# Kernel optimization log

Measured on AMD Instinct MI355X. Metric: run time of the kernel, lower is better.

Reference implementation:

```python
import jax, jax.numpy as jnp
import numpy as np

D_MODEL = 1024
N_HEADS = 16
HEAD_DIM = D_MODEL // N_HEADS
FFN_DIM = 4096
T = 2048
LN_EPS = 1e-5


def layer_norm(x, g, b):
    mu = jnp.mean(x, axis=-1, keepdims=True)
    var = jnp.mean(jnp.square(x - mu), axis=-1, keepdims=True)
    return (x - mu) * jax.lax.rsqrt(var + LN_EPS) * g + b


def setup_inputs() -> dict:
    key = jax.random.key(0)
    ks = jax.random.split(key, 12)
    s = 0.02
    x = jax.random.normal(ks[0], (1, T, D_MODEL), dtype=jnp.float32)
    # causal mask: True means masked (strict upper triangle)
    causal_mask = jnp.triu(jnp.ones((T, T), dtype=bool), k=1)
    # ALiBi bias: -slope * distance, per head
    slopes = 2.0 ** (-8.0 * (jnp.arange(1, N_HEADS + 1, dtype=jnp.float32) / N_HEADS))
    pos = jnp.arange(T, dtype=jnp.float32)
    dist = pos[None, :] - pos[:, None]  # (T, T)
    alibi_bias = slopes[:, None, None] * jnp.minimum(dist, 0.0)[None]  # (H, T, T)
    inp = {
        "x": x,
        "causal_mask": causal_mask,
        "alibi_bias": alibi_bias.astype(jnp.float32),
        "wq": jax.random.normal(ks[1], (D_MODEL, D_MODEL), jnp.float32) * s,
        "bq": jnp.zeros((D_MODEL,), jnp.float32),
        "wk": jax.random.normal(ks[2], (D_MODEL, D_MODEL), jnp.float32) * s,
        "bk": jnp.zeros((D_MODEL,), jnp.float32),
        "wv": jax.random.normal(ks[3], (D_MODEL, D_MODEL), jnp.float32) * s,
        "bv": jnp.zeros((D_MODEL,), jnp.float32),
        "wo": jax.random.normal(ks[4], (D_MODEL, D_MODEL), jnp.float32) * s,
        "bo": jnp.zeros((D_MODEL,), jnp.float32),
        "w1": jax.random.normal(ks[5], (D_MODEL, FFN_DIM), jnp.float32) * s,
        "b1": jnp.zeros((FFN_DIM,), jnp.float32),
        "w2": jax.random.normal(ks[6], (FFN_DIM, D_MODEL), jnp.float32) * s,
        "b2": jnp.zeros((D_MODEL,), jnp.float32),
        "g1": jnp.ones((D_MODEL,), jnp.float32),
        "be1": jnp.zeros((D_MODEL,), jnp.float32),
        "g2": jnp.ones((D_MODEL,), jnp.float32),
        "be2": jnp.zeros((D_MODEL,), jnp.float32),
    }
    return inp


def reference(x, causal_mask, alibi_bias, wq, bq, wk, bk, wv, bv, wo, bo,
              w1, b1, w2, b2, g1, be1, g2, be2):
    B, Tt, D = x.shape
    H, hd = N_HEADS, HEAD_DIM
    x_norm = layer_norm(x, g1, be1)
    # projections -> (B, H, T, hd)
    def split_heads(y):
        return y.reshape(B, Tt, H, hd).transpose(0, 2, 1, 3)
    Q = split_heads(x_norm @ wq + bq)
    K = split_heads(x_norm @ wk + bk)
    V = split_heads(x_norm @ wv + bv)
    scale = jnp.sqrt(jnp.float32(hd))
    scores = jnp.einsum('bhqd,bhkd->bhqk', Q, K) / scale
    scores = scores + alibi_bias[None]
    scores = jnp.where(causal_mask[None, None], -jnp.inf, scores)
    attn = jax.nn.softmax(scores, axis=-1)
    attn_out = jnp.einsum('bhqk,bhkd->bhqd', attn, V)
    attn_out = attn_out.transpose(0, 2, 1, 3).reshape(B, Tt, D)
    attn_out = attn_out @ wo + bo
    x = x + attn_out
    x_norm = layer_norm(x, g2, be2)
    h = jax.nn.gelu(x_norm @ w1 + b1, approximate=False)
    ffn_out = h @ w2 + b2
    return x + ffn_out
```

## Files before the change

kernel.cpp:

```cpp
#include <hip/hip_runtime.h>
#include <hip/hip_bf16.h>
#include <math.h>

#define T_SEQ 2048
#define D_MODEL 1024
#define N_HEADS 16
#define HEAD_DIM 64
#define FFN_DIM 4096

typedef _Float16 halfx8 __attribute__((ext_vector_type(8)));
typedef _Float16 halfx4 __attribute__((ext_vector_type(4)));
typedef float floatx4 __attribute__((ext_vector_type(4)));

__device__ __forceinline__ void async_ld16(const _Float16* g, _Float16* l) {
  __builtin_amdgcn_global_load_lds(
      (const __attribute__((address_space(1))) unsigned int*)g,
      (__attribute__((address_space(3))) unsigned int*)l, 16, 0, 0);
}

template <int N> __device__ __forceinline__ void wait_barrier();
template <> __device__ __forceinline__ void wait_barrier<0>() {
  asm volatile("s_waitcnt vmcnt(0)\n\ts_barrier" ::: "memory");
}
template <> __device__ __forceinline__ void wait_barrier<2>() {
  asm volatile("s_waitcnt vmcnt(2)\n\ts_barrier" ::: "memory");
}
template <> __device__ __forceinline__ void wait_barrier<3>() {
  asm volatile("s_waitcnt vmcnt(3)\n\ts_barrier" ::: "memory");
}
template <> __device__ __forceinline__ void wait_barrier<4>() {
  asm volatile("s_waitcnt vmcnt(4)\n\ts_barrier" ::: "memory");
}

#define DPP_STEP(v, CTRL, OP)                                                 \
  {                                                                           \
    float _t = __int_as_float(__builtin_amdgcn_update_dpp(                    \
        0, __float_as_int(v), CTRL, 0xF, 0xF, true));                         \
    (v) = OP((v), _t);                                                        \
  }
#define OP_MAXF(a, b) fmaxf((a), (b))
#define OP_ADDF(a, b) ((a) + (b))

__global__ __launch_bounds__(256) void prep_ln_kernel(
    const float* __restrict__ wq, const float* __restrict__ wk,
    const float* __restrict__ wv, const float* __restrict__ wo,
    const float* __restrict__ w1, const float* __restrict__ w2,
    const float* __restrict__ bq, const float* __restrict__ bk,
    const float* __restrict__ bv, _Float16* __restrict__ Wqkvt,
    _Float16* __restrict__ Wot, _Float16* __restrict__ W1t,
    _Float16* __restrict__ W2t, float* __restrict__ bqkv,
    const float* __restrict__ x, const float* __restrict__ g1,
    const float* __restrict__ be1, _Float16* __restrict__ xnh) {
  int bId = blockIdx.x;
  int tid = threadIdx.x;
  if (bId >= 12300) {
    int row = bId - 12300;
    const float* xr = x + (size_t)row * D_MODEL;
    _Float16* yr = xnh + (size_t)row * D_MODEL;
    int lid = tid & 63, wid = tid >> 6;
    __shared__ float red[8];
    float4 v = *(const float4*)&xr[tid * 4];
    float sum = v.x + v.y + v.z + v.w;
    for (int o = 32; o > 0; o >>= 1) sum += __shfl_down(sum, o, 64);
    if (lid == 0) red[wid] = sum;
    __syncthreads();
    if (tid == 0) { float t = 0; for (int i = 0; i < 4; i++) t += red[i]; red[0] = t; }
    __syncthreads();
    float mu = red[0] * (1.0f / D_MODEL);
    __syncthreads();
    float dx = v.x - mu, dy = v.y - mu, dz = v.z - mu, dw = v.w - mu;
    float vs = dx * dx + dy * dy + dz * dz + dw * dw;
    for (int o = 32; o > 0; o >>= 1) vs += __shfl_down(vs, o, 64);
    if (lid == 0) red[wid] = vs;
    __syncthreads();
    if (tid == 0) { float t = 0; for (int i = 0; i < 4; i++) t += red[i]; red[0] = t; }
    __syncthreads();
    float rstd = rsqrtf(red[0] * (1.0f / D_MODEL) + 1e-5f);
    float4 gv = *(const float4*)&g1[tid * 4];
    float4 bv4 = *(const float4*)&be1[tid * 4];
    halfx4 o;
    o[0] = (_Float16)(dx * rstd * gv.x + bv4.x);
    o[1] = (_Float16)(dy * rstd * gv.y + bv4.y);
    o[2] = (_Float16)(dz * rstd * gv.z + bv4.z);
    o[3] = (_Float16)(dw * rstd * gv.w + bv4.w);
    *(halfx4*)&yr[tid * 4] = o;
    return;
  }
  if (bId >= 12288) {
    int i = (bId - 12288) * 256 + tid;
    if (i < 1024) bqkv[i] = bq[i];
    else if (i < 2048) bqkv[i] = bk[i - 1024];
    else bqkv[i] = bv[i - 2048];
    return;
  }
  const float* in; _Float16* outp; int K, N, t;
  if (bId < 1024)      { in = wq; outp = Wqkvt;                 K = 1024; N = 1024; t = bId; }
  else if (bId < 2048) { in = wk; outp = Wqkvt + 1024 * 1024;   K = 1024; N = 1024; t = bId - 1024; }
  else if (bId < 3072) { in = wv; outp = Wqkvt + 2 * 1024 * 1024; K = 1024; N = 1024; t = bId - 2048; }
  else if (bId < 4096) { in = wo; outp = Wot;                   K = 1024; N = 1024; t = bId - 3072; }
  else if (bId < 8192) { in = w1; outp = W1t;                   K = 1024; N = 4096; t = bId - 4096; }
  else                 { in = w2; outp = W2t;                   K = 4096; N = 1024; t = bId - 8192; }
  int ntn = N / 32;
  int tk = (t / ntn) * 32, tn = (t % ntn) * 32;

  __shared__ float tile[32][33];
  int r = tid >> 3, c = (tid & 7) * 4;
  float4 v = *(const float4*)&in[(size_t)(tk + r) * N + tn + c];
  tile[r][c] = v.x; tile[r][c + 1] = v.y; tile[r][c + 2] = v.z; tile[r][c + 3] = v.w;
  __syncthreads();
  halfx4 o;
  o[0] = (_Float16)tile[c][r];
  o[1] = (_Float16)tile[c + 1][r];
  o[2] = (_Float16)tile[c + 2][r];
  o[3] = (_Float16)tile[c + 3][r];
  *(halfx4*)&outp[(size_t)(tn + r) * K + tk + c] = o;
}

__global__ __launch_bounds__(256) void ln_h_kernel(
    const float* __restrict__ x, const float* __restrict__ g,
    const float* __restrict__ b, _Float16* __restrict__ y) {
  int row = blockIdx.x;
  const float* xr = x + (size_t)row * D_MODEL;
  _Float16* yr = y + (size_t)row * D_MODEL;
  int tid = threadIdx.x;
  int lid = tid & 63, wid = tid >> 6;
  __shared__ float red[8];

  float4 v = *(const float4*)&xr[tid * 4];
  float sum = v.x + v.y + v.z + v.w;
  for (int o = 32; o > 0; o >>= 1) sum += __shfl_down(sum, o, 64);
  if (lid == 0) red[wid] = sum;
  __syncthreads();
  if (tid == 0) { float t = 0; for (int i = 0; i < 4; i++) t += red[i]; red[0] = t; }
  __syncthreads();
  float mu = red[0] * (1.0f / D_MODEL);
  __syncthreads();

  float dx = v.x - mu, dy = v.y - mu, dz = v.z - mu, dw = v.w - mu;
  float vs = dx * dx + dy * dy + dz * dz + dw * dw;
  for (int o = 32; o > 0; o >>= 1) vs += __shfl_down(vs, o, 64);
  if (lid == 0) red[wid] = vs;
  __syncthreads();
  if (tid == 0) { float t = 0; for (int i = 0; i < 4; i++) t += red[i]; red[0] = t; }
  __syncthreads();
  float rstd = rsqrtf(red[0] * (1.0f / D_MODEL) + 1e-5f);

  float4 gv = *(const float4*)&g[tid * 4];
  float4 bv = *(const float4*)&b[tid * 4];
  halfx4 o;
  o[0] = (_Float16)(dx * rstd * gv.x + bv.x);
  o[1] = (_Float16)(dy * rstd * gv.y + bv.y);
  o[2] = (_Float16)(dz * rstd * gv.z + bv.z);
  o[3] = (_Float16)(dw * rstd * gv.w + bv.w);
  *(halfx4*)&yr[tid * 4] = o;
}

template <int MODE, int BM, int BN>
__global__ __launch_bounds__(256) void hgemm_kernel(
    const _Float16* __restrict__ A, const _Float16* __restrict__ Bt,
    const float* __restrict__ bias, const float* __restrict__ res,
    float* __restrict__ Cf, _Float16* __restrict__ Ch,
    _Float16* __restrict__ Vtg, int M, int N, int K) {
  constexpr int TM = BM / 32;
  constexpr int TN = BN / 32;
  constexpr int AR = BM / 64;
  constexpr int BR = BN / 64;
  constexpr int L = AR + BR;
  __shared__ _Float16 As[3][BM][32];
  __shared__ _Float16 Bs[3][BN][32];
  const int tid = threadIdx.x;
  const int w = tid >> 6, lane = tid & 63;
  const int l16 = lane & 15, quad = lane >> 4;
  const int m0 = blockIdx.y * BM, n0 = blockIdx.x * BN;
  const int wm = (w >> 1) * (BM / 2), wn = (w & 1) * (BN / 2);

  floatx4 acc[TM][TN];
#pragma unroll
  for (int i = 0; i < TM; i++)
#pragma unroll
    for (int j = 0; j < TN; j++) acc[i][j] = (floatx4){0.f, 0.f, 0.f, 0.f};

  const int srow = w * 16 + (lane >> 2);
  const int gg = (lane & 3) ^ ((srow >> 1) & 3);
  const _Float16* Agp = A + (size_t)(m0 + srow) * K + gg * 8;
  const _Float16* Bgp = Bt + (size_t)(n0 + srow) * K + gg * 8;

  const int colA = (quad ^ ((l16 >> 1) & 3)) * 8;

  const int NIT = K / 32;
#define HG_ISSUE(buf, k0)                                                     \
  {                                                                           \
    _Pragma("unroll") for (int i = 0; i < AR; i++)                            \
        async_ld16(Agp + (k0) + (size_t)i * 64 * K, &As[buf][i * 64 + w * 16][0]); \
    _Pragma("unroll") for (int i = 0; i < BR; i++)                            \
        async_ld16(Bgp + (k0) + (size_t)i * 64 * K, &Bs[buf][i * 64 + w * 16][0]); \
  }
  HG_ISSUE(0, 0)
  HG_ISSUE(1, 32)

  for (int it = 0; it < NIT; it++) {
    const int buf = it % 3;
    if (it + 1 < NIT) wait_barrier<L>();
    else wait_barrier<0>();
    if (it + 2 < NIT) HG_ISSUE((it + 2) % 3, (it + 2) * 32)
    halfx8 af[TM], bf[TN];
#pragma unroll
    for (int mt = 0; mt < TM; mt++)
      af[mt] = *(const halfx8*)&As[buf][wm + mt * 16 + l16][colA];
#pragma unroll
    for (int nt = 0; nt < TN; nt++)
      bf[nt] = *(const halfx8*)&Bs[buf][wn + nt * 16 + l16][colA];
#pragma unroll
    for (int mt = 0; mt < TM; mt++)
#pragma unroll
      for (int nt = 0; nt < TN; nt++)
        acc[mt][nt] = __builtin_amdgcn_mfma_f32_16x16x32_f16(af[mt], bf[nt], acc[mt][nt], 0, 0, 0);
  }

#pragma unroll
  for (int mt = 0; mt < TM; mt++) {
    int row0 = m0 + wm + mt * 16 + quad * 4;
#pragma unroll
    for (int nt = 0; nt < TN; nt++) {
      int col = n0 + wn + nt * 16 + l16;
      float bv = bias[col];
      float vv[4];
#pragma unroll
      for (int r = 0; r < 4; r++) {
        float v = acc[mt][nt][r] + bv;
        if (MODE == 1) v = 0.5f * v * (1.0f + erff(v * 0.70710678118f));
        vv[r] = v;
      }
      if (MODE == 2) {
#pragma unroll
        for (int r = 0; r < 4; r++)
          Cf[(size_t)(row0 + r) * N + col] = vv[r] + res[(size_t)(row0 + r) * N + col];
      } else if (MODE == 3) {
        if (col < 2048) {
#pragma unroll
          for (int r = 0; r < 4; r++)
            Ch[(size_t)(row0 + r) * 2048 + col] = (_Float16)vv[r];
        } else {
          halfx4 pk;
#pragma unroll
          for (int r = 0; r < 4; r++) pk[r] = (_Float16)vv[r];
          *(halfx4*)&Vtg[(size_t)(col - 2048) * T_SEQ + row0] = pk;
        }
      } else {
#pragma unroll
        for (int r = 0; r < 4; r++)
          Ch[(size_t)(row0 + r) * N + col] = (_Float16)vv[r];
      }
    }
  }
}

#define LROW 72
__global__ __launch_bounds__(256) void flash_attn_kernel(
    const _Float16* __restrict__ QK, const _Float16* __restrict__ Vtg,
    _Float16* __restrict__ out) {
  __shared__ _Float16 Ks[2][64][64];
  __shared__ _Float16 Vt[2][64][64];
  __shared__ _Float16 Ps[4][16][LROW];

  const int h = blockIdx.y;
  const int qt = 31 - blockIdx.x;
  const int q0 = qt * 64;
  const int tid = threadIdx.x;
  const int w = tid >> 6;
  const int lane = tid & 63;
  const int l16 = lane & 15;
  const int quad = lane >> 4;

  const _Float16* Qg = QK + h * HEAD_DIM;
  const _Float16* Kg = QK + 1024 + h * HEAD_DIM;
  const _Float16* Vg = Vtg + (size_t)h * HEAD_DIM * T_SEQ;

  const _Float16* qp = Qg + (size_t)(q0 + w * 16 + l16) * 2048;
  halfx8 qa0 = *(const halfx8*)(qp + quad * 8);
  halfx8 qa1 = *(const halfx8*)(qp + 32 + quad * 8);

  const float scale2 = 0.18033688f;
  const float slope2 = exp2f(-0.5f * (float)(h + 1)) * 1.44269504f;
  const int row_base = q0 + w * 16 + quad * 4;

  const int sr = w * 8 + (lane >> 3);
  const int gg = (lane & 7) ^ ((lane >> 3) & 7);
  const _Float16* Kp = Kg + (size_t)sr * 2048 + gg * 8;
  const _Float16* Vp = Vg + (size_t)sr * 2048 + gg * 8;

  const int m7 = l16 & 7;
  const int cK0 = (quad ^ m7) * 8;
  const int cK1 = cK0 ^ 32;
  const int cV0 = (quad ^ m7) * 8;
  const int cV1 = ((quad + 4) ^ m7) * 8;

#define FA_ISSUE(buf, k0)                                                      \
  {                                                                            \
    async_ld16(Kp + (size_t)(k0) * 2048, &Ks[buf][w * 8][0]);                  \
    async_ld16(Kp + (size_t)((k0) + 32) * 2048, &Ks[buf][32 + w * 8][0]);      \
    async_ld16(Vp + (k0), &Vt[buf][w * 8][0]);                                 \
    async_ld16(Vp + (size_t)32 * 2048 + (k0), &Vt[buf][32 + w * 8][0]);        \
  }

  float m_i[4], l_i[4];
  floatx4 o_acc[4];
#pragma unroll
  for (int r = 0; r < 4; r++) { m_i[r] = -INFINITY; l_i[r] = 0.f; }
#pragma unroll
  for (int c = 0; c < 4; c++) o_acc[c] = (floatx4){0.f, 0.f, 0.f, 0.f};

  FA_ISSUE(0, 0)

  for (int t = 0; t <= qt; t++) {
    const int k0 = t * 64;
    const int buf = t & 1;
    wait_barrier<0>();
    if (t < qt) FA_ISSUE(buf ^ 1, k0 + 64)

    float sc[4][4];
#pragma unroll
    for (int sub = 0; sub < 4; sub++) {
      const _Float16* kr = &Ks[buf][sub * 16 + l16][0];
      halfx8 b0 = *(const halfx8*)(kr + cK0);
      halfx8 b1 = *(const halfx8*)(kr + cK1);
      floatx4 acc = (floatx4){0.f, 0.f, 0.f, 0.f};
      acc = __builtin_amdgcn_mfma_f32_16x16x32_f16(qa0, b0, acc, 0, 0, 0);
      acc = __builtin_amdgcn_mfma_f32_16x16x32_f16(qa1, b1, acc, 0, 0, 0);
#pragma unroll
      for (int r = 0; r < 4; r++) sc[sub][r] = acc[r];
    }

    const bool diag = (t == qt);
    float mx[4];
#pragma unroll
    for (int r = 0; r < 4; r++) {
      const int rg = row_base + r;
      float ab = slope2 * (float)(k0 + l16 - rg);
      mx[r] = m_i[r];
#pragma unroll
      for (int sub = 0; sub < 4; sub++) {
        float s = sc[sub][r] * scale2 + (ab + slope2 * (float)(sub * 16));
        if (diag && (k0 + sub * 16 + l16) > rg) s = -1e30f;
        sc[sub][r] = s;
        mx[r] = fmaxf(mx[r], s);
      }
    }
#pragma unroll
    for (int r = 0; r < 4; r++) DPP_STEP(mx[r], 0x121, OP_MAXF)
#pragma unroll
    for (int r = 0; r < 4; r++) DPP_STEP(mx[r], 0x122, OP_MAXF)
#pragma unroll
    for (int r = 0; r < 4; r++) DPP_STEP(mx[r], 0x124, OP_MAXF)
#pragma unroll
    for (int r = 0; r < 4; r++) DPP_STEP(mx[r], 0x128, OP_MAXF)

    float ls[4], alpha[4];
#pragma unroll
    for (int r = 0; r < 4; r++) {
      alpha[r] = exp2f(m_i[r] - mx[r]);
      m_i[r] = mx[r];
      float l = 0.f;
#pragma unroll
      for (int sub = 0; sub < 4; sub++) {
        float p = exp2f(sc[sub][r] - mx[r]);
        l += p;
        Ps[w][quad * 4 + r][sub * 16 + l16] = (_Float16)p;
      }
      ls[r] = l;
    }
#pragma unroll
    for (int r = 0; r < 4; r++) DPP_STEP(ls[r], 0x121, OP_ADDF)
#pragma unroll
    for (int r = 0; r < 4; r++) DPP_STEP(ls[r], 0x122, OP_ADDF)
#pragma unroll
    for (int r = 0; r < 4; r++) DPP_STEP(ls[r], 0x124, OP_ADDF)
#pragma unroll
    for (int r = 0; r < 4; r++) DPP_STEP(ls[r], 0x128, OP_ADDF)
#pragma unroll
    for (int r = 0; r < 4; r++) {
      l_i[r] = l_i[r] * alpha[r] + ls[r];
#pragma unroll
      for (int c = 0; c < 4; c++) o_acc[c][r] *= alpha[r];
    }

#pragma unroll
    for (int kh = 0; kh < 2; kh++) {
      halfx8 pa = *(const halfx8*)(&Ps[w][l16][kh * 32 + quad * 8]);
      const int cV = kh ? cV1 : cV0;
#pragma unroll
      for (int c = 0; c < 4; c++) {
        halfx8 vb = *(const halfx8*)(&Vt[buf][c * 16 + l16][cV]);
        o_acc[c] = __builtin_amdgcn_mfma_f32_16x16x32_f16(pa, vb, o_acc[c], 0, 0, 0);
      }
    }
  }

#pragma unroll
  for (int c = 0; c < 4; c++)
#pragma unroll
    for (int r = 0; r < 4; r++)
      out[(size_t)(row_base + r) * D_MODEL + h * HEAD_DIM + c * 16 + l16] =
          (_Float16)(o_acc[c][r] / l_i[r]);
}

extern "C" void kernel_launch(void* const* d_in, const int* in_sizes, int n_in,
                              void* d_out, int out_size, void* d_ws, size_t ws_size,
                              hipStream_t stream) {
  const float* x   = (const float*)d_in[0];
  const float* wq  = (const float*)d_in[3];
  const float* bq  = (const float*)d_in[4];
  const float* wk  = (const float*)d_in[5];
  const float* bk  = (const float*)d_in[6];
  const float* wv  = (const float*)d_in[7];
  const float* bv  = (const float*)d_in[8];
  const float* wo  = (const float*)d_in[9];
  const float* bo  = (const float*)d_in[10];
  const float* w1  = (const float*)d_in[11];
  const float* b1  = (const float*)d_in[12];
  const float* w2  = (const float*)d_in[13];
  const float* b2  = (const float*)d_in[14];
  const float* g1  = (const float*)d_in[15];
  const float* be1 = (const float*)d_in[16];
  const float* g2  = (const float*)d_in[17];
  const float* be2 = (const float*)d_in[18];
  float* out = (float*)d_out;

  const size_t TD = (size_t)T_SEQ * D_MODEL;
  char* p = (char*)d_ws;
  float*    x1    = (float*)p;     p += TD * 4;
  float*    bqkv  = (float*)p;     p += 4096 * 4;
  _Float16* xnh   = (_Float16*)p;  p += TD * 2;
  _Float16* QKh   = (_Float16*)p;  p += (size_t)2048 * 2048 * 2;
  _Float16* Vtg   = (_Float16*)p;  p += (size_t)1024 * 2048 * 2;
  _Float16* attnh = (_Float16*)p;  p += TD * 2;
  _Float16* hh    = (_Float16*)p;  p += (size_t)2048 * 4096 * 2;
  _Float16* Wqkvt = (_Float16*)p;  p += (size_t)3 * 1024 * 1024 * 2;
  _Float16* Wot   = (_Float16*)p;  p += (size_t)1024 * 1024 * 2;
  _Float16* W1t   = (_Float16*)p;  p += (size_t)1024 * 4096 * 2;
  _Float16* W2t   = (_Float16*)p;  p += (size_t)4096 * 1024 * 2;

  dim3 blk(256);

  prep_ln_kernel<<<dim3(12300 + T_SEQ), blk, 0, stream>>>(
      wq, wk, wv, wo, w1, w2, bq, bk, bv, Wqkvt, Wot, W1t, W2t, bqkv,
      x, g1, be1, xnh);

  hgemm_kernel<3, 128, 128><<<dim3(3072 / 128, T_SEQ / 128), blk, 0, stream>>>(
      xnh, Wqkvt, bqkv, nullptr, nullptr, QKh, Vtg, T_SEQ, 3072, 1024);

  flash_attn_kernel<<<dim3(T_SEQ / 64, N_HEADS), blk, 0, stream>>>(QKh, Vtg, attnh);

  hgemm_kernel<2, 64, 64><<<dim3(1024 / 64, T_SEQ / 64), blk, 0, stream>>>(
      attnh, Wot, bo, x, x1, nullptr, nullptr, T_SEQ, 1024, 1024);

  ln_h_kernel<<<T_SEQ, blk, 0, stream>>>(x1, g2, be2, xnh);

  hgemm_kernel<1, 128, 128><<<dim3(4096 / 128, T_SEQ / 128), blk, 0, stream>>>(
      xnh, W1t, b1, nullptr, nullptr, hh, nullptr, T_SEQ, 4096, 1024);

  hgemm_kernel<2, 64, 64><<<dim3(1024 / 64, T_SEQ / 64), blk, 0, stream>>>(
      hh, W2t, b2, x1, out, nullptr, nullptr, T_SEQ, 1024, 4096);
}
```

Measured before the change: 563.1 us.

## Split long causal attention query tiles across two blocks and merge partials

The upper half of query tiles (qt 16-31) is now split into two key ranges, each handled by a separate block that writes unnormalized fp32 partial outputs plus running max and sum. A new combine kernel merges the two partials with log-sum-exp rescaling and writes fp16 output. The goal is to balance per-block work in the causal flash attention and shorten the tail caused by the longest tiles. In exchange it adds an extra kernel launch and fp32 partial traffic through the workspace.

```diff
diff --git a/kernel.cpp b/kernel.cpp
--- a/kernel.cpp
+++ b/kernel.cpp
@@ -258,13 +258,27 @@
 #define LROW 72
 __global__ __launch_bounds__(256) void flash_attn_kernel(
     const _Float16* __restrict__ QK, const _Float16* __restrict__ Vtg,
-    _Float16* __restrict__ out) {
+    _Float16* __restrict__ out, float* __restrict__ Opart,
+    float* __restrict__ Mpart, float* __restrict__ Lpart) {
   __shared__ _Float16 Ks[2][64][64];
   __shared__ _Float16 Vt[2][64][64];
   __shared__ _Float16 Ps[4][16][LROW];
 
   const int h = blockIdx.y;
-  const int qt = 31 - blockIdx.x;
+  const int bx = blockIdx.x;
+  int qt, tlo, thi, split;
+  if (bx < 32) {
+    qt = 31 - (bx >> 1);
+    split = bx & 1;
+    int nt = qt + 1, nt1 = nt >> 1;
+    tlo = split ? nt1 : 0;
+    thi = split ? nt : nt1;
+  } else {
+    qt = 47 - bx;
+    split = -1;
+    tlo = 0;
+    thi = qt + 1;
+  }
   const int q0 = qt * 64;
   const int tid = threadIdx.x;
   const int w = tid >> 6;
@@ -310,13 +324,13 @@
 #pragma unroll
   for (int c = 0; c < 4; c++) o_acc[c] = (floatx4){0.f, 0.f, 0.f, 0.f};
 
-  FA_ISSUE(0, 0)
-
-  for (int t = 0; t <= qt; t++) {
+  FA_ISSUE(0, tlo * 64)
+
+  for (int t = tlo; t < thi; t++) {
     const int k0 = t * 64;
-    const int buf = t & 1;
+    const int buf = (t - tlo) & 1;
     wait_barrier<0>();
-    if (t < qt) FA_ISSUE(buf ^ 1, k0 + 64)
+    if (t + 1 < thi) FA_ISSUE(buf ^ 1, (t + 1) * 64)
 
     float sc[4][4];
 #pragma unroll
@@ -396,12 +410,50 @@
     }
   }
 
-#pragma unroll
-  for (int c = 0; c < 4; c++)
-#pragma unroll
-    for (int r = 0; r < 4; r++)
-      out[(size_t)(row_base + r) * D_MODEL + h * HEAD_DIM + c * 16 + l16] =
-          (_Float16)(o_acc[c][r] / l_i[r]);
+  if (split < 0) {
+#pragma unroll
+    for (int c = 0; c < 4; c++)
+#pragma unroll
+      for (int r = 0; r < 4; r++)
+        out[(size_t)(row_base + r) * D_MODEL + h * HEAD_DIM + c * 16 + l16] =
+            (_Float16)(o_acc[c][r] / l_i[r]);
+  } else {
+    float* Ob = Opart + (((size_t)split * 16 + h) * 1024) * 64;
+#pragma unroll
+    for (int r = 0; r < 4; r++) {
+      int qrel = row_base + r - 1024;
+#pragma unroll
+      for (int c = 0; c < 4; c++)
+        Ob[(size_t)qrel * 64 + c * 16 + l16] = o_acc[c][r];
+      if (l16 == 0) {
+        int pq = split * 16384 + h * 1024 + qrel;
+        Mpart[pq] = m_i[r];
+        Lpart[pq] = l_i[r];
+      }
+    }
+  }
+}
+
+__global__ __launch_bounds__(256) void fa_combine_kernel(
+    const float* __restrict__ Opart, const float* __restrict__ Mpart,
+    const float* __restrict__ Lpart, _Float16* __restrict__ out) {
+  int g = blockIdx.x * 256 + threadIdx.x;
+  int d4 = (g & 15) * 4;
+  int q = (g >> 4) & 1023;
+  int h = g >> 14;
+  int pq = h * 1024 + q;
+  float m0 = Mpart[pq], m1 = Mpart[16384 + pq];
+  float l0 = Lpart[pq], l1 = Lpart[16384 + pq];
+  float M = fmaxf(m0, m1);
+  float a0 = exp2f(m0 - M), a1 = exp2f(m1 - M);
+  float inv = 1.0f / (a0 * l0 + a1 * l1);
+  const float* O0 = Opart + ((size_t)h * 1024 + q) * 64 + d4;
+  const float* O1 = O0 + (size_t)16 * 1024 * 64;
+  halfx4 o;
+#pragma unroll
+  for (int j = 0; j < 4; j++)
+    o[j] = (_Float16)((a0 * O0[j] + a1 * O1[j]) * inv);
+  *(halfx4*)&out[(size_t)(q + 1024) * D_MODEL + h * HEAD_DIM + d4] = o;
 }
 
 extern "C" void kernel_launch(void* const* d_in, const int* in_sizes, int n_in,
@@ -439,6 +491,9 @@
   _Float16* Wot   = (_Float16*)p;  p += (size_t)1024 * 1024 * 2;
   _Float16* W1t   = (_Float16*)p;  p += (size_t)1024 * 4096 * 2;
   _Float16* W2t   = (_Float16*)p;  p += (size_t)4096 * 1024 * 2;
+  float*    Opart = (float*)p;     p += (size_t)2 * 16 * 1024 * 64 * 4;
+  float*    Mpart = (float*)p;     p += (size_t)2 * 16 * 1024 * 4;
+  float*    Lpart = (float*)p;     p += (size_t)2 * 16 * 1024 * 4;
 
   dim3 blk(256);
 
@@ -449,7 +504,9 @@
   hgemm_kernel<3, 128, 128><<<dim3(3072 / 128, T_SEQ / 128), blk, 0, stream>>>(
       xnh, Wqkvt, bqkv, nullptr, nullptr, QKh, Vtg, T_SEQ, 3072, 1024);
 
-  flash_attn_kernel<<<dim3(T_SEQ / 64, N_HEADS), blk, 0, stream>>>(QKh, Vtg, attnh);
+  flash_attn_kernel<<<dim3(48, N_HEADS), blk, 0, stream>>>(
+      QKh, Vtg, attnh, Opart, Mpart, Lpart);
+  fa_combine_kernel<<<dim3(1024), blk, 0, stream>>>(Opart, Mpart, Lpart, attnh);
 
   hgemm_kernel<2, 64, 64><<<dim3(1024 / 64, T_SEQ / 64), blk, 0, stream>>>(
       attnh, Wot, bo, x, x1, nullptr, nullptr, T_SEQ, 1024, 1024);
```

Measured after the change: 550.6 us. -2.2%, faster.
